# Kernel tuning notes

Hardware: AMD Instinct MI355X
Metric: run time of the kernel (lower is better)

## Reference

```python
import jax, jax.numpy as jnp
import numpy as np

B, T, C = 2, 2048, 1024
NH = 16

def setup_inputs() -> dict:
    key = jax.random.key(0)
    ks = jax.random.split(key, 5)
    s = 0.02
    return {
        "x": jax.random.normal(ks[0], (B, T, C), dtype=jnp.float32),
        "w_attn": jax.random.normal(ks[1], (C, 3 * C), dtype=jnp.float32) * s,
        "b_attn": jax.random.normal(ks[2], (3 * C,), dtype=jnp.float32) * s,
        "w_proj": jax.random.normal(ks[3], (C, C), dtype=jnp.float32) * s,
        "b_proj": jax.random.normal(ks[4], (C,), dtype=jnp.float32) * s,
        "n_heads": NH,
    }

def reference(x, w_attn, b_attn, w_proj, b_proj, n_heads):
    Bx, Tx, Cx = x.shape
    hd = Cx // n_heads
    qkv = x @ w_attn + b_attn                      # [B,T,3C]
    q, k, v = jnp.split(qkv, 3, axis=-1)
    # [B,T,H,hd] -> [B,H,T,hd]
    q = q.reshape(Bx, Tx, n_heads, hd).transpose(0, 2, 1, 3)
    k = k.reshape(Bx, Tx, n_heads, hd).transpose(0, 2, 1, 3)
    v = v.reshape(Bx, Tx, n_heads, hd).transpose(0, 2, 1, 3)
    scale = 1.0 / np.sqrt(hd).astype(np.float32)
    att = jnp.einsum('bhqd,bhkd->bhqk', q, k) * scale   # [B,H,T,T]
    causal = jnp.tril(jnp.ones((Tx, Tx), dtype=bool))
    att = jnp.where(causal[None, None], att, -jnp.inf)
    att = jax.nn.softmax(att, axis=-1)
    y = jnp.einsum('bhqk,bhkd->bhqd', att, v)            # [B,H,T,hd]
    y = y.transpose(0, 2, 1, 3).reshape(Bx, Tx, Cx)
    return y @ w_proj + b_proj
```

## Files before the change

kernel.cpp:

```cpp
#include <hip/hip_runtime.h>

typedef __bf16 bf16x8 __attribute__((ext_vector_type(8)));
typedef __bf16 bf16x4 __attribute__((ext_vector_type(4)));
typedef float  f32x4  __attribute__((ext_vector_type(4)));

#define MFMA_BF16(a, b, c) __builtin_amdgcn_mfma_f32_16x16x32_bf16((a), (b), (c), 0, 0, 0)
#define NEG_INF (-1e30f)
#define SCL 0.18033688f

__device__ __forceinline__ void gld16(const void* g, void* l) {
  __builtin_amdgcn_global_load_lds(
      (const __attribute__((address_space(1))) void*)g,
      (__attribute__((address_space(3))) void*)l, 16, 0, 0);
}

__global__ void cast_f32_bf16(const float* __restrict__ in,
                              __bf16* __restrict__ out, int n) {
  int i = (blockIdx.x * 256 + threadIdx.x) * 8;
  if (i >= n) return;
  float4 a = *(const float4*)&in[i];
  float4 b = *(const float4*)&in[i + 4];
  bf16x8 v;
  v[0] = (__bf16)a.x; v[1] = (__bf16)a.y; v[2] = (__bf16)a.z; v[3] = (__bf16)a.w;
  v[4] = (__bf16)b.x; v[5] = (__bf16)b.y; v[6] = (__bf16)b.z; v[7] = (__bf16)b.w;
  *(bf16x8*)&out[i] = v;
}

__global__ void transpose_f32_bf16(const float* __restrict__ in,
                                   __bf16* __restrict__ out, int R, int C) {
  __shared__ float t[32][33];
  int tx = threadIdx.x & 31, ty = threadIdx.x >> 5;
  int x = blockIdx.x * 32 + tx;
  int y0 = blockIdx.y * 32 + ty;
#pragma unroll
  for (int i = 0; i < 4; ++i)
    t[ty + 8 * i][tx] = in[(size_t)(y0 + 8 * i) * C + x];
  __syncthreads();
  int x2 = blockIdx.y * 32 + tx;
#pragma unroll
  for (int i = 0; i < 4; ++i)
    out[(size_t)(blockIdx.x * 32 + ty + 8 * i) * R + x2] = (__bf16)t[tx][ty + 8 * i];
}

__global__ void transpose_v(const __bf16* __restrict__ qkv,
                            __bf16* __restrict__ vt) {
  __shared__ __bf16 t[32][33];
  int tx = threadIdx.x & 31, ty = threadIdx.x >> 5;
  int bh = blockIdx.z, b = bh >> 4, h = bh & 15;
  int t0 = blockIdx.x * 32, d0 = blockIdx.y * 32;
#pragma unroll
  for (int i = 0; i < 4; ++i)
    t[ty + 8 * i][tx] =
        qkv[(size_t)(b * 2048 + t0 + ty + 8 * i) * 3072 + 2048 + h * 64 + d0 + tx];
  __syncthreads();
#pragma unroll
  for (int i = 0; i < 4; ++i)
    vt[(size_t)(bh * 64 + d0 + ty + 8 * i) * 2048 + t0 + tx] = t[tx][ty + 8 * i];
}

#define BN 128
#define BK 64

template <int BMT, typename TC>
__global__ __launch_bounds__(256) void gemm_bt_bias(
    const __bf16* __restrict__ A, const __bf16* __restrict__ Bt,
    const float* __restrict__ bias, TC* __restrict__ Cmat,
    int M, int N, int K) {
  constexpr int NI = BMT / 32;
  __shared__ __align__(16) __bf16 As[BMT * BK];
  __shared__ __align__(16) __bf16 Bs[BN * BK];
  int tid = threadIdx.x;
  int wave = tid >> 6, lane = tid & 63;
  int l16 = lane & 15, quad = lane >> 4;
  int wm = wave >> 1, wn = wave & 1;
  int m0 = blockIdx.y * BMT, n0 = blockIdx.x * BN;

  f32x4 acc[NI][4];
#pragma unroll
  for (int i = 0; i < NI; ++i)
#pragma unroll
    for (int j = 0; j < 4; ++j) acc[i][j] = (f32x4){0.f, 0.f, 0.f, 0.f};

  int row = tid >> 3;
  int kc = ((tid & 7) ^ ((tid >> 3) & 7)) * 8;
  int xr = (l16 & 7) * 8;

  for (int k0 = 0; k0 < K; k0 += BK) {
#pragma unroll
    for (int i = 0; i < NI; ++i)
      gld16(&A[(size_t)(m0 + row + i * 32) * K + k0 + kc],
            (char*)As + (i * 256 + wave * 64) * 16);
#pragma unroll
    for (int j = 0; j < 4; ++j)
      gld16(&Bt[(size_t)(n0 + row + j * 32) * K + k0 + kc],
            (char*)Bs + (j * 256 + wave * 64) * 16);
    __syncthreads();
#pragma unroll
    for (int ks = 0; ks < 2; ++ks) {
      bf16x8 af[NI], bfr[4];
#pragma unroll
      for (int i = 0; i < NI; ++i)
        af[i] = *(const bf16x8*)&As[(wm * (BMT / 2) + i * 16 + l16) * BK +
                                    ((ks * 32 + quad * 8) ^ xr)];
#pragma unroll
      for (int j = 0; j < 4; ++j)
        bfr[j] = *(const bf16x8*)&Bs[(wn * 64 + j * 16 + l16) * BK +
                                     ((ks * 32 + quad * 8) ^ xr)];
#pragma unroll
      for (int i = 0; i < NI; ++i)
#pragma unroll
        for (int j = 0; j < 4; ++j) acc[i][j] = MFMA_BF16(af[i], bfr[j], acc[i][j]);
    }
    __syncthreads();
  }
#pragma unroll
  for (int i = 0; i < NI; ++i) {
#pragma unroll
    for (int j = 0; j < 4; ++j) {
      int col = n0 + wn * 64 + j * 16 + l16;
      float bv = bias[col];
#pragma unroll
      for (int r = 0; r < 4; ++r) {
        int rw = m0 + wm * (BMT / 2) + i * 16 + quad * 4 + r;
        Cmat[(size_t)rw * N + col] = (TC)(acc[i][j][r] + bv);
      }
    }
  }
}

__global__ __launch_bounds__(256) void attn_causal(
    const __bf16* __restrict__ qkv, const __bf16* __restrict__ vt,
    __bf16* __restrict__ y) {
  __shared__ __align__(16) __bf16 Kb[2][64 * 64];
  __shared__ __align__(16) __bf16 Vb[2][64 * 64];
  __shared__ __align__(16) __bf16 Ps[4][16 * 72];
  const int tid = threadIdx.x;
  const int wave = tid >> 6, lane = tid & 63;
  const int l16 = lane & 15, quad = lane >> 4;
  const int bh = blockIdx.x;
  const int b = bh >> 4, h = bh & 15;
  const int RS = 3072;

  const int row0 = tid >> 3;
  const int kcs = ((tid & 7) ^ ((tid >> 3) & 7)) * 8;
  const int xr = (l16 & 7) * 8;
  const __bf16* kbase = qkv + (size_t)(b * 2048) * RS + 1024 + h * 64 + kcs;
  const __bf16* vbase = vt + (size_t)(bh * 64) * 2048 + kcs;

#pragma unroll 1
  for (int phase = 0; phase < 2; ++phase) {
    const int qt = phase ? (31 - (int)blockIdx.y) : (int)blockIdx.y;

    int qrow = b * 2048 + qt * 64 + wave * 16 + l16;
    const __bf16* qbase = qkv + (size_t)qrow * RS + h * 64;
    bf16x8 qf0 = *(const bf16x8*)(qbase + quad * 8);
    bf16x8 qf1 = *(const bf16x8*)(qbase + 32 + quad * 8);

    float l_i = 0.f;
    f32x4 o[4];
#pragma unroll
    for (int j = 0; j < 4; ++j) o[j] = (f32x4){0.f, 0.f, 0.f, 0.f};

#pragma unroll
    for (int i = 0; i < 2; ++i) {
      gld16(kbase + (size_t)(row0 + 32 * i) * RS,
            (char*)Kb[0] + (i * 256 + tid) * 16);
      gld16(vbase + (size_t)(row0 + 32 * i) * 2048,
            (char*)Vb[0] + (i * 256 + tid) * 16);
    }
    __syncthreads();

    for (int kt = 0; kt <= qt; ++kt) {
      const int cur = kt & 1;
      if (kt < qt) {
#pragma unroll
        for (int i = 0; i < 2; ++i) {
          gld16(kbase + (size_t)((kt + 1) * 64 + row0 + 32 * i) * RS,
                (char*)Kb[cur ^ 1] + (i * 256 + tid) * 16);
          gld16(vbase + (size_t)(row0 + 32 * i) * 2048 + (kt + 1) * 64,
                (char*)Vb[cur ^ 1] + (i * 256 + tid) * 16);
        }
      }

      f32x4 s[4];
#pragma unroll
      for (int j = 0; j < 4; ++j) s[j] = (f32x4){0.f, 0.f, 0.f, 0.f};
#pragma unroll
      for (int j = 0; j < 4; ++j) {
        bf16x8 kf0 = *(const bf16x8*)&Kb[cur][(j * 16 + l16) * 64 + ((quad * 8) ^ xr)];
        bf16x8 kf1 = *(const bf16x8*)&Kb[cur][(j * 16 + l16) * 64 + ((32 + quad * 8) ^ xr)];
        s[j] = MFMA_BF16(kf0, qf0, s[j]);
        s[j] = MFMA_BF16(kf1, qf1, s[j]);
      }

      if (kt == qt) {
        int qg = wave * 16 + l16;
#pragma unroll
        for (int j = 0; j < 4; ++j)
#pragma unroll
          for (int r = 0; r < 4; ++r)
            if (j * 16 + quad * 4 + r > qg) s[j][r] = NEG_INF;
      }

#pragma unroll
      for (int j = 0; j < 4; ++j) {
        bf16x4 pb;
#pragma unroll
        for (int r = 0; r < 4; ++r) {
          float p = __builtin_amdgcn_exp2f(s[j][r] * SCL);
          l_i += p;
          pb[r] = (__bf16)p;
        }
        *(bf16x4*)&Ps[wave][l16 * 72 + j * 16 + quad * 4] = pb;
      }

#pragma unroll
      for (int ks = 0; ks < 2; ++ks) {
        bf16x8 pf = *(const bf16x8*)&Ps[wave][l16 * 72 + ks * 32 + quad * 8];
#pragma unroll
        for (int j = 0; j < 4; ++j) {
          bf16x8 vf = *(const bf16x8*)&Vb[cur][(j * 16 + l16) * 64 +
                                              ((ks * 32 + quad * 8) ^ xr)];
          o[j] = MFMA_BF16(pf, vf, o[j]);
        }
      }
      __syncthreads();
    }

    float lred = l_i;
    lred += __shfl_xor(lred, 16);
    lred += __shfl_xor(lred, 32);
    int orow = b * 2048 + qt * 64 + wave * 16 + quad * 4;
#pragma unroll
    for (int r = 0; r < 4; ++r) {
      float inv = 1.f / __shfl(lred, quad * 4 + r);
#pragma unroll
      for (int j = 0; j < 4; ++j)
        y[(size_t)(orow + r) * 1024 + h * 64 + j * 16 + l16] = (__bf16)(o[j][r] * inv);
    }
  }
}

extern "C" void kernel_launch(void* const* d_in, const int* in_sizes, int n_in,
                              void* d_out, int out_size, void* d_ws, size_t ws_size,
                              hipStream_t stream) {
  (void)in_sizes; (void)n_in; (void)out_size; (void)ws_size;
  const float* x      = (const float*)d_in[0];
  const float* w_attn = (const float*)d_in[1];
  const float* b_attn = (const float*)d_in[2];
  const float* w_proj = (const float*)d_in[3];
  const float* b_proj = (const float*)d_in[4];
  float* out = (float*)d_out;

  __bf16* wt_attn = (__bf16*)d_ws;
  __bf16* wt_proj = wt_attn + (size_t)3072 * 1024;
  __bf16* qkv     = wt_proj + (size_t)1024 * 1024;
  __bf16* ybuf    = qkv + (size_t)4096 * 3072;
  __bf16* vtbuf   = ybuf + (size_t)4096 * 1024;

  cast_f32_bf16<<<4096 * 1024 / 2048, 256, 0, stream>>>(x, ybuf, 4096 * 1024);

  transpose_f32_bf16<<<dim3(3072 / 32, 1024 / 32), 256, 0, stream>>>(w_attn, wt_attn, 1024, 3072);
  transpose_f32_bf16<<<dim3(1024 / 32, 1024 / 32), 256, 0, stream>>>(w_proj, wt_proj, 1024, 1024);

  gemm_bt_bias<128, __bf16><<<dim3(3072 / BN, 4096 / 128), 256, 0, stream>>>(
      ybuf, wt_attn, b_attn, qkv, 4096, 3072, 1024);

  transpose_v<<<dim3(64, 2, 32), 256, 0, stream>>>(qkv, vtbuf);

  attn_causal<<<dim3(2 * 16, 16), 256, 0, stream>>>(qkv, vtbuf, ybuf);

  gemm_bt_bias<64, float><<<dim3(1024 / BN, 4096 / 64), 256, 0, stream>>>(
      ybuf, wt_proj, b_proj, out, 4096, 1024, 1024);
}
```

Measured before the change: 182.5 us.

## Replace QKV GEMM with 8-phase pipelined 256x192 kernel writing V transposed

Replaces the QKV projection GEMM with a new 512-thread kernel that uses 256x192 tiles and double-buffered LDS loaded through direct global-to-LDS copies. The main loop is split into eight phases that interleave MFMA work with prefetches, using explicit barriers, waitcnt and setprio. The epilogue writes V straight into the transposed layout, so the separate transpose_v kernel is removed. This trades more complex hand scheduling and strided bf16x4 stores of V for fewer launches and better overlap of memory and MFMA work.

```diff
diff --git a/kernel.cpp b/kernel.cpp
--- a/kernel.cpp
+++ b/kernel.cpp
@@ -40,22 +40,6 @@
 #pragma unroll
   for (int i = 0; i < 4; ++i)
     out[(size_t)(blockIdx.x * 32 + ty + 8 * i) * R + x2] = (__bf16)t[tx][ty + 8 * i];
-}
-
-__global__ void transpose_v(const __bf16* __restrict__ qkv,
-                            __bf16* __restrict__ vt) {
-  __shared__ __bf16 t[32][33];
-  int tx = threadIdx.x & 31, ty = threadIdx.x >> 5;
-  int bh = blockIdx.z, b = bh >> 4, h = bh & 15;
-  int t0 = blockIdx.x * 32, d0 = blockIdx.y * 32;
-#pragma unroll
-  for (int i = 0; i < 4; ++i)
-    t[ty + 8 * i][tx] =
-        qkv[(size_t)(b * 2048 + t0 + ty + 8 * i) * 3072 + 2048 + h * 64 + d0 + tx];
-  __syncthreads();
-#pragma unroll
-  for (int i = 0; i < 4; ++i)
-    vt[(size_t)(bh * 64 + d0 + ty + 8 * i) * 2048 + t0 + tx] = t[tx][ty + 8 * i];
 }
 
 #define BN 128
@@ -128,6 +112,124 @@
   }
 }
 
+#define BARX do { asm volatile("" ::: "memory"); __builtin_amdgcn_s_barrier(); \
+                  asm volatile("" ::: "memory"); } while (0)
+#define WLGKM do { asm volatile("s_waitcnt lgkmcnt(0)" ::: "memory"); \
+                   __builtin_amdgcn_sched_barrier(0); } while (0)
+#define WVM4 asm volatile("s_waitcnt vmcnt(4)" ::: "memory")
+#define STA8(SBUF, SKS, T) do { \
+    gld16(srcA1 + (size_t)(T) * 64 + (SKS) * 32, (char*)&As[SBUF][SKS][0] + tid * 16); \
+    gld16(srcA2 + (size_t)(T) * 64 + (SKS) * 32, (char*)&As[SBUF][SKS][0] + tid * 16 + 8192); \
+  } while (0)
+#define STB8(SBUF, SKS, T) do { \
+    gld16(srcB1 + (size_t)(T) * 64 + (SKS) * 32, (char*)&Bs[SBUF][SKS][0] + tid * 16); \
+    gld16(srcB2 + (size_t)(T) * 64 + (SKS) * 32, (char*)&Bs[SBUF][SKS][0] + tid * 16 + 8192); \
+  } while (0)
+#define LDA4(CBUF, CKS, MQ) do { \
+    const __bf16* p_ = &As[CBUF][CKS][(wm * 128 + (MQ) * 64 + l16) * 32 + xrd]; \
+    af[0] = *(const bf16x8*)(p_);        af[1] = *(const bf16x8*)(p_ + 512); \
+    af[2] = *(const bf16x8*)(p_ + 1024); af[3] = *(const bf16x8*)(p_ + 1536); \
+  } while (0)
+#define LDB3(CBUF, CKS) do { \
+    const __bf16* p_ = &Bs[CBUF][CKS][(wn * 48 + l16) * 32 + xrd]; \
+    bfr[0] = *(const bf16x8*)(p_);       bfr[1] = *(const bf16x8*)(p_ + 512); \
+    bfr[2] = *(const bf16x8*)(p_ + 1024); \
+  } while (0)
+#define MM12(MQ) do { \
+    __builtin_amdgcn_s_setprio(1); \
+    _Pragma("unroll") for (int mi_ = 0; mi_ < 4; ++mi_) \
+    _Pragma("unroll") for (int nj_ = 0; nj_ < 3; ++nj_) \
+      acc[(MQ) * 4 + mi_][nj_] = MFMA_BF16(af[mi_], bfr[nj_], acc[(MQ) * 4 + mi_][nj_]); \
+    __builtin_amdgcn_s_setprio(0); \
+  } while (0)
+
+__global__ __launch_bounds__(512, 2) void gemm_qkv_8ph(
+    const __bf16* __restrict__ A, const __bf16* __restrict__ Bt,
+    const float* __restrict__ bias, __bf16* __restrict__ qkv,
+    __bf16* __restrict__ vt) {
+  constexpr int GK = 1024, GN = 3072, NT = 16;
+  __shared__ __align__(16) __bf16 As[2][2][256 * 32];
+  __shared__ __align__(16) __bf16 Bs[2][2][256 * 32];
+  const int tid = threadIdx.x;
+  const int wave = tid >> 6, lane = tid & 63;
+  const int l16 = lane & 15, quad = lane >> 4;
+  const int wm = wave >> 2, wn = wave & 3;
+  const int m0 = blockIdx.y * 256, n0 = blockIdx.x * 192;
+
+  const int row0 = tid >> 2;
+  const int kc = (((tid & 3) ^ ((row0 >> 1) & 3)) * 8);
+  const int xrd = (quad ^ ((l16 >> 1) & 3)) * 8;
+
+  const __bf16* srcA1 = A + (size_t)(m0 + row0) * GK + kc;
+  const __bf16* srcA2 = srcA1 + (size_t)128 * GK;
+  const __bf16* srcB1 = Bt + (size_t)(n0 + row0) * GK + kc;
+  const int br2 = (row0 + 128 < 192) ? row0 + 128 : 191;
+  const __bf16* srcB2 = Bt + (size_t)(n0 + br2) * GK + kc;
+
+  f32x4 acc[8][3];
+#pragma unroll
+  for (int m = 0; m < 8; ++m)
+#pragma unroll
+    for (int n = 0; n < 3; ++n) acc[m][n] = (f32x4){0.f, 0.f, 0.f, 0.f};
+
+  STA8(0, 0, 0); STB8(0, 0, 0);
+  STA8(0, 1, 0); STB8(0, 1, 0);
+  STA8(1, 0, 1); STB8(1, 0, 1);
+  WVM4;
+  BARX;
+
+  bf16x8 af[4], bfr[3];
+#pragma unroll 1
+  for (int i = 0; i < NT / 2; ++i) {
+    const int v = 2 * i + 1;
+    const int t2 = (2 * i + 2 < NT) ? 2 * i + 2 : NT - 1;
+    const int t3 = (2 * i + 3 < NT) ? 2 * i + 3 : NT - 1;
+    LDA4(0, 0, 0); LDB3(0, 0); STA8(1, 1, v);
+    BARX; WLGKM; MM12(0); BARX;
+    LDA4(0, 0, 1); STB8(1, 1, v);
+    BARX; WLGKM; MM12(1); BARX;
+    LDA4(0, 1, 0); LDB3(0, 1); STA8(0, 0, t2);
+    BARX; WLGKM; MM12(0); BARX;
+    LDA4(0, 1, 1); STB8(0, 0, t2);
+    BARX; WLGKM; MM12(1); WVM4; BARX;
+    LDA4(1, 0, 0); LDB3(1, 0); STA8(0, 1, t2);
+    BARX; WLGKM; MM12(0); BARX;
+    LDA4(1, 0, 1); STB8(0, 1, t2);
+    BARX; WLGKM; MM12(1); BARX;
+    LDA4(1, 1, 0); LDB3(1, 1); STA8(1, 0, t3);
+    BARX; WLGKM; MM12(0); BARX;
+    LDA4(1, 1, 1); STB8(1, 0, t3);
+    BARX; WLGKM; MM12(1); WVM4; BARX;
+  }
+
+#pragma unroll
+  for (int n = 0; n < 3; ++n) {
+    const int c0 = n0 + wn * 48 + n * 16;
+    const int col = c0 + l16;
+    const float bv = bias[col];
+    if (c0 < 2048) {
+#pragma unroll
+      for (int m = 0; m < 8; ++m) {
+        const int rw = m0 + wm * 128 + m * 16 + quad * 4;
+#pragma unroll
+        for (int r = 0; r < 4; ++r)
+          qkv[(size_t)(rw + r) * GN + col] = (__bf16)(acc[m][n][r] + bv);
+      }
+    } else {
+      const int h = (col - 2048) >> 6, d = col & 63;
+#pragma unroll
+      for (int m = 0; m < 8; ++m) {
+        const int t0 = m0 + wm * 128 + m * 16 + quad * 4;
+        const int b = t0 >> 11, tt = t0 & 2047;
+        bf16x4 pb;
+#pragma unroll
+        for (int r = 0; r < 4; ++r) pb[r] = (__bf16)(acc[m][n][r] + bv);
+        *(bf16x4*)&vt[(size_t)((b * 16 + h) * 64 + d) * 2048 + tt] = pb;
+      }
+    }
+  }
+}
+
 __global__ __launch_bounds__(256) void attn_causal(
     const __bf16* __restrict__ qkv, const __bf16* __restrict__ vt,
     __bf16* __restrict__ y) {
@@ -263,10 +365,8 @@
   transpose_f32_bf16<<<dim3(3072 / 32, 1024 / 32), 256, 0, stream>>>(w_attn, wt_attn, 1024, 3072);
   transpose_f32_bf16<<<dim3(1024 / 32, 1024 / 32), 256, 0, stream>>>(w_proj, wt_proj, 1024, 1024);
 
-  gemm_bt_bias<128, __bf16><<<dim3(3072 / BN, 4096 / 128), 256, 0, stream>>>(
-      ybuf, wt_attn, b_attn, qkv, 4096, 3072, 1024);
-
-  transpose_v<<<dim3(64, 2, 32), 256, 0, stream>>>(qkv, vtbuf);
+  gemm_qkv_8ph<<<dim3(3072 / 192, 4096 / 256), 512, 0, stream>>>(
+      ybuf, wt_attn, b_attn, qkv, vtbuf);
 
   attn_causal<<<dim3(2 * 16, 16), 256, 0, stream>>>(qkv, vtbuf, ybuf);
 
```

Result: faster. 176.5 us (-3.3%).
